# Kernel optimization log

Measured on AMD Instinct MI355X. Metric: run time of the kernel, lower is better.

The kernel has to match this reference:

```python
import jax, jax.numpy as jnp
import numpy as np

P_THRESH = 20  # p=0.2 * 100
# direction -> (di, dj): masked pixel (i,j) writes input[i,j] to x[i+di, j+dj], then avg to x[i,j]
OFFSETS = {0: (-1, -1), 1: (-1, 0), 2: (-1, 1), 3: (0, -1), 4: (0, 0), 5: (0, 1), 6: (1, -1), 7: (1, 0)}


def _shift(a, di, dj):
    """out[i+di, j+dj] = a[i, j] on last two axes; out-of-range -> 0/False."""
    H, W = a.shape[-2], a.shape[-1]
    pad = [(0, 0)] * (a.ndim - 2) + [(max(di, 0), max(-di, 0)), (max(dj, 0), max(-dj, 0))]
    p = jnp.pad(a, pad)
    sh, sw = max(-di, 0), max(-dj, 0)
    return p[..., sh:sh + H, sw:sw + W]


def _avg3x3_reflect(x):
    H, W = x.shape[-2], x.shape[-1]
    p = jnp.pad(x, [(0, 0), (0, 0), (1, 1), (1, 1)], mode='reflect')
    s = jnp.zeros_like(x)
    for i in range(3):
        for j in range(3):
            s = s + p[..., i:i + H, j:j + W]
    return s / 9.0


def brown_forward(input, dir, prob):
    avg = _avg3x3_reflect(input)
    pos = prob <= P_THRESH
    x = input
    for d in range(8):  # sequential, matching torch in-place write order
        di, dj = OFFSETS[d]
        m = (dir == d) & pos
        if d == 4:
            x = jnp.where(m, avg, x)  # mm: only avg write
        else:
            sm = _shift(m, di, dj)                       # neighbor-target mask
            x = jnp.where(sm, _shift(input, di, dj), x)  # x[i+di,j+dj] = input[i,j]
            mv = _shift(sm, -di, -dj)                    # mask restricted to valid region
            x = jnp.where(mv, avg, x)                    # x[i,j] = avg[i,j]
    return x


def setup_inputs() -> dict:
    key = jax.random.key(0)
    k1, k2, k3 = jax.random.split(key, 3)
    shape = (32, 64, 128, 128)
    return {
        'input': jax.random.normal(k1, shape, dtype=jnp.float32),
        'dir': jax.random.randint(k2, shape, 0, 8, dtype=jnp.int32),
        'prob': jax.random.randint(k3, shape, 1, 100, dtype=jnp.int32),
    }


def reference(input, dir, prob):
    return brown_forward(input, dir, prob)
```

## Files before the change

kernel.cpp:

```cpp
#include <hip/hip_runtime.h>
#include <cstddef>

#define H 128
#define W 128
#define P_THRESH 20

typedef float f4u __attribute__((ext_vector_type(4), aligned(4)));
typedef int   i4u __attribute__((ext_vector_type(4), aligned(4)));
typedef float nf2 __attribute__((ext_vector_type(2)));

__global__ __launch_bounds__(256, 6)
void brown_kernel(const float* __restrict__ inp,
                  const int*  __restrict__ dirp,
                  const int*  __restrict__ prb,
                  float* __restrict__ out)
{
    const int tid  = threadIdx.x;
    const int lane = tid & 63;
    const int bid  = blockIdx.x;
    const int slice = bid >> 5;
    const int gi   = ((bid & 31) << 2) | (tid >> 6);
    const size_t base = (size_t)slice * (size_t)(H * W);

    const int j0 = lane << 1;
    const int cl = (lane == 0) ? 0 : ((lane == 63) ? (W - 4) : (j0 - 1));

    const int rT = (gi == 0) ? 1 : gi - 1;
    const int rB = (gi == H - 1) ? H - 2 : gi + 1;

    const float* ip = inp  + base;
    const int*   dp = dirp + base;
    const int*   pp = prb  + base;

    const f4u iT = *(const f4u*)(ip + (size_t)rT * W + cl);
    const f4u iM = *(const f4u*)(ip + (size_t)gi * W + cl);
    const f4u iB = *(const f4u*)(ip + (size_t)rB * W + cl);
    const i4u dT = *(const i4u*)(dp + (size_t)rT * W + cl);
    const i4u dM = *(const i4u*)(dp + (size_t)gi * W + cl);
    const i4u dB = *(const i4u*)(dp + (size_t)rB * W + cl);
    const i4u pT = *(const i4u*)(pp + (size_t)rT * W + cl);
    const i4u pM = *(const i4u*)(pp + (size_t)gi * W + cl);
    const i4u pB = *(const i4u*)(pp + (size_t)rB * W + cl);

    auto packm = [](i4u d, i4u p) -> unsigned {
        const unsigned a = (p.x <= P_THRESH) ? (unsigned)d.x : 8u;
        const unsigned b = (p.y <= P_THRESH) ? (unsigned)d.y : 8u;
        const unsigned c = (p.z <= P_THRESH) ? (unsigned)d.z : 8u;
        const unsigned e = (p.w <= P_THRESH) ? (unsigned)d.w : 8u;
        return a | (b << 8) | (c << 16) | (e << 24);
    };
    unsigned mT = packm(dT, pT);
    unsigned mM = packm(dM, pM);
    unsigned mB = packm(dB, pB);

    if (gi == 0) {
        mT = 0x08080808u;
        unsigned r = 0;
        #pragma unroll
        for (int i2 = 0; i2 < 4; ++i2) {
            unsigned b = (mM >> (8 * i2)) & 255u;
            b = (b <= 2u) ? 8u : b;
            r |= b << (8 * i2);
        }
        mM = r;
    } else if (gi == H - 1) {
        mB = 0x08080808u;
        unsigned r = 0;
        #pragma unroll
        for (int i2 = 0; i2 < 4; ++i2) {
            unsigned b = (mM >> (8 * i2)) & 255u;
            b = (b >= 6u) ? 8u : b;
            r |= b << (8 * i2);
        }
        mM = r;
    }

    float vT[4] = {iT.x, iT.y, iT.z, iT.w};
    float vM[4] = {iM.x, iM.y, iM.z, iM.w};
    float vB[4] = {iB.x, iB.y, iB.z, iB.w};
    if (lane == 0) {
        vT[0] = iT.y; vT[1] = iT.x; vT[2] = iT.y; vT[3] = iT.z;
        vM[0] = iM.y; vM[1] = iM.x; vM[2] = iM.y; vM[3] = iM.z;
        vB[0] = iB.y; vB[1] = iB.x; vB[2] = iB.y; vB[3] = iB.z;
        mT = (mT << 8) | 8u;
        mB = (mB << 8) | 8u;
        mM = (mM << 8) | 8u;
        const unsigned b1 = (mM >> 8) & 255u;
        if ((0x49u >> b1) & 1u) mM = (mM & ~0xFF00u) | (8u << 8);
    } else if (lane == 63) {
        vT[0] = iT.y; vT[1] = iT.z; vT[2] = iT.w; vT[3] = iT.z;
        vM[0] = iM.y; vM[1] = iM.z; vM[2] = iM.w; vM[3] = iM.z;
        vB[0] = iB.y; vB[1] = iB.z; vB[2] = iB.w; vB[3] = iB.z;
        mT = (mT >> 8) | 0x08000000u;
        mB = (mB >> 8) | 0x08000000u;
        mM = (mM >> 8) | 0x08000000u;
        const unsigned b2 = (mM >> 16) & 255u;
        if ((0x24u >> b2) & 1u) mM = (mM & ~0xFF0000u) | (8u << 16);
    }

    float cs[4];
    #pragma unroll
    for (int w = 0; w < 4; ++w) cs[w] = vT[w] + vM[w] + vB[w];

    nf2 res;
    #pragma unroll
    for (int p = 0; p < 2; ++p) {
        const float avg = (cs[p] + cs[p + 1] + cs[p + 2]) * (1.0f / 9.0f);
        const unsigned wT = mT >> (8 * p);
        const unsigned wM = mM >> (8 * p);
        const unsigned wB = mB >> (8 * p);

        float val = vM[p + 1];
        int dl = -1;
        if (((wB >> 16) & 255u) == 0u) { val = vB[p + 2]; dl = 0; }
        if (((wB >>  8) & 255u) == 1u) { val = vB[p + 1]; dl = 1; }
        if (( wB        & 255u) == 2u) { val = vB[p];     dl = 2; }
        if (((wM >> 16) & 255u) == 3u) { val = vM[p + 2]; dl = 3; }
        if (( wM        & 255u) == 5u) { val = vM[p];     dl = 5; }
        if (((wT >> 16) & 255u) == 6u) { val = vT[p + 2]; dl = 6; }
        if (((wT >>  8) & 255u) == 7u) { val = vT[p + 1]; dl = 7; }

        const int msel = (int)((wM >> 8) & 255u);
        if ((msel < 8) & (msel >= dl)) val = avg;
        res[p] = val;
    }
    *(nf2*)(out + base + (size_t)gi * W + j0) = res;
}

extern "C" void kernel_launch(void* const* d_in, const int* in_sizes, int n_in,
                              void* d_out, int out_size, void* d_ws, size_t ws_size,
                              hipStream_t stream) {
    const float* inp  = (const float*)d_in[0];
    const int*   dirp = (const int*)d_in[1];
    const int*   prb  = (const int*)d_in[2];
    float* out = (float*)d_out;

    const int slices = in_sizes[0] / (H * W);
    const int grid = slices * 32;
    brown_kernel<<<grid, 256, 0, stream>>>(inp, dirp, prb, out);
}
```

Measured before the change: 397.2 us.

## Stage packed dir/prob masks in shared memory to cut redundant halo loads

Each block now loads the dir and prob rows it needs (its 4 rows plus one halo row above and below) once, with coalesced 16-byte loads, and packs them into byte masks in LDS. Threads then read their 3x3 mask neighborhood from shared memory instead of each thread re-reading three overlapping rows of dir and prob from global memory. Boundary and edge-lane handling moves into the packing stage, and edge-lane value shuffles become branchless selects. Launch bounds are raised to 8 blocks per CU. This cuts redundant global traffic and instruction count, at the cost of a __syncthreads and some unaligned LDS reads.

```diff
diff --git a/kernel.cpp b/kernel.cpp
--- a/kernel.cpp
+++ b/kernel.cpp
@@ -9,93 +9,103 @@
 typedef int   i4u __attribute__((ext_vector_type(4), aligned(4)));
 typedef float nf2 __attribute__((ext_vector_type(2)));
 
-__global__ __launch_bounds__(256, 6)
+__global__ __launch_bounds__(256, 8)
 void brown_kernel(const float* __restrict__ inp,
                   const int*  __restrict__ dirp,
                   const int*  __restrict__ prb,
                   float* __restrict__ out)
 {
-    const int tid  = threadIdx.x;
-    const int lane = tid & 63;
-    const int bid  = blockIdx.x;
+    __shared__ unsigned int s_mk[1 + 6 * 33];
+
+    const int tid   = threadIdx.x;
+    const int bid   = blockIdx.x;
     const int slice = bid >> 5;
-    const int gi   = ((bid & 31) << 2) | (tid >> 6);
+    const int r0    = (bid & 31) << 2;
     const size_t base = (size_t)slice * (size_t)(H * W);
 
-    const int j0 = lane << 1;
+    const int lane = tid & 63;
+    const int row  = tid >> 6;
+    const int gi   = r0 + row;
+    const int j0   = lane << 1;
+
     const int cl = (lane == 0) ? 0 : ((lane == 63) ? (W - 4) : (j0 - 1));
-
     const int rT = (gi == 0) ? 1 : gi - 1;
     const int rB = (gi == H - 1) ? H - 2 : gi + 1;
-
-    const float* ip = inp  + base;
-    const int*   dp = dirp + base;
-    const int*   pp = prb  + base;
-
+    const float* ip = inp + base;
     const f4u iT = *(const f4u*)(ip + (size_t)rT * W + cl);
     const f4u iM = *(const f4u*)(ip + (size_t)gi * W + cl);
     const f4u iB = *(const f4u*)(ip + (size_t)rB * W + cl);
-    const i4u dT = *(const i4u*)(dp + (size_t)rT * W + cl);
-    const i4u dM = *(const i4u*)(dp + (size_t)gi * W + cl);
-    const i4u dB = *(const i4u*)(dp + (size_t)rB * W + cl);
-    const i4u pT = *(const i4u*)(pp + (size_t)rT * W + cl);
-    const i4u pM = *(const i4u*)(pp + (size_t)gi * W + cl);
-    const i4u pB = *(const i4u*)(pp + (size_t)rB * W + cl);
 
-    auto packm = [](i4u d, i4u p) -> unsigned {
-        const unsigned a = (p.x <= P_THRESH) ? (unsigned)d.x : 8u;
-        const unsigned b = (p.y <= P_THRESH) ? (unsigned)d.y : 8u;
-        const unsigned c = (p.z <= P_THRESH) ? (unsigned)d.z : 8u;
-        const unsigned e = (p.w <= P_THRESH) ? (unsigned)d.w : 8u;
-        return a | (b << 8) | (c << 16) | (e << 24);
-    };
-    unsigned mT = packm(dT, pT);
-    unsigned mM = packm(dM, pM);
-    unsigned mB = packm(dB, pB);
+    if (tid < 192) {
+        const int r6 = tid >> 5;
+        const int w  = tid & 31;
+        const int gr = r0 + r6 - 1;
+        unsigned m;
+        if ((unsigned)gr < (unsigned)H) {
+            const i4u dv = *(const i4u*)(dirp + base + (size_t)gr * W + 4 * w);
+            const i4u pv = *(const i4u*)(prb  + base + (size_t)gr * W + 4 * w);
+            const unsigned a = (pv.x <= P_THRESH) ? (unsigned)dv.x : 8u;
+            const unsigned b = (pv.y <= P_THRESH) ? (unsigned)dv.y : 8u;
+            const unsigned c = (pv.z <= P_THRESH) ? (unsigned)dv.z : 8u;
+            const unsigned e = (pv.w <= P_THRESH) ? (unsigned)dv.w : 8u;
+            m = a | (b << 8) | (c << 16) | (e << 24);
+            if (gr == 0) {
+                unsigned mm = 0;
+                #pragma unroll
+                for (int i2 = 0; i2 < 4; ++i2) {
+                    unsigned bb = (m >> (8 * i2)) & 255u;
+                    bb = (bb <= 2u) ? 8u : bb;
+                    mm |= bb << (8 * i2);
+                }
+                m = mm;
+            } else if (gr == H - 1) {
+                unsigned mm = 0;
+                #pragma unroll
+                for (int i2 = 0; i2 < 4; ++i2) {
+                    unsigned bb = (m >> (8 * i2)) & 255u;
+                    bb = (bb >= 6u) ? 8u : bb;
+                    mm |= bb << (8 * i2);
+                }
+                m = mm;
+            }
+            if (w == 0) {
+                const unsigned b0 = m & 255u;
+                if ((0x49u >> b0) & 1u) m = (m & ~255u) | 8u;
+            }
+            if (w == 31) {
+                const unsigned b3 = m >> 24;
+                if ((0x24u >> b3) & 1u) m = (m & 0x00FFFFFFu) | (8u << 24);
+            }
+        } else {
+            m = 0x08080808u;
+        }
+        s_mk[1 + 33 * r6 + w] = m;
+        if (w == 31) s_mk[1 + 33 * r6 + 32] = 0x08080808u;
+    } else if (tid == 192) {
+        s_mk[0] = 0x08080808u;
+    }
+    __syncthreads();
 
-    if (gi == 0) {
-        mT = 0x08080808u;
-        unsigned r = 0;
-        #pragma unroll
-        for (int i2 = 0; i2 < 4; ++i2) {
-            unsigned b = (mM >> (8 * i2)) & 255u;
-            b = (b <= 2u) ? 8u : b;
-            r |= b << (8 * i2);
-        }
-        mM = r;
-    } else if (gi == H - 1) {
-        mB = 0x08080808u;
-        unsigned r = 0;
-        #pragma unroll
-        for (int i2 = 0; i2 < 4; ++i2) {
-            unsigned b = (mM >> (8 * i2)) & 255u;
-            b = (b >= 6u) ? 8u : b;
-            r |= b << (8 * i2);
-        }
-        mM = r;
+    unsigned mrow[3];
+    #pragma unroll
+    for (int dr = 0; dr < 3; ++dr) {
+        const int addr = 132 * (row + dr) + (j0 + 3);
+        const unsigned w0 = s_mk[addr >> 2];
+        const unsigned w1 = s_mk[(addr >> 2) + 1];
+        const int sh = 8 * (addr & 3);
+        mrow[dr] = (w0 >> sh) | (w1 << (32 - sh));
     }
+    const unsigned mT = mrow[0], mM = mrow[1], mB = mrow[2];
 
-    float vT[4] = {iT.x, iT.y, iT.z, iT.w};
-    float vM[4] = {iM.x, iM.y, iM.z, iM.w};
-    float vB[4] = {iB.x, iB.y, iB.z, iB.w};
-    if (lane == 0) {
-        vT[0] = iT.y; vT[1] = iT.x; vT[2] = iT.y; vT[3] = iT.z;
-        vM[0] = iM.y; vM[1] = iM.x; vM[2] = iM.y; vM[3] = iM.z;
-        vB[0] = iB.y; vB[1] = iB.x; vB[2] = iB.y; vB[3] = iB.z;
-        mT = (mT << 8) | 8u;
-        mB = (mB << 8) | 8u;
-        mM = (mM << 8) | 8u;
-        const unsigned b1 = (mM >> 8) & 255u;
-        if ((0x49u >> b1) & 1u) mM = (mM & ~0xFF00u) | (8u << 8);
-    } else if (lane == 63) {
-        vT[0] = iT.y; vT[1] = iT.z; vT[2] = iT.w; vT[3] = iT.z;
-        vM[0] = iM.y; vM[1] = iM.z; vM[2] = iM.w; vM[3] = iM.z;
-        vB[0] = iB.y; vB[1] = iB.z; vB[2] = iB.w; vB[3] = iB.z;
-        mT = (mT >> 8) | 0x08000000u;
-        mB = (mB >> 8) | 0x08000000u;
-        mM = (mM >> 8) | 0x08000000u;
-        const unsigned b2 = (mM >> 16) & 255u;
-        if ((0x24u >> b2) & 1u) mM = (mM & ~0xFF0000u) | (8u << 16);
+    const bool e0 = (lane == 0), e63 = (lane == 63), eE = e0 | e63;
+    float vT[4], vM[4], vB[4];
+    {
+        vT[0] = eE ? iT.y : iT.x;  vT[1] = e0 ? iT.x : (e63 ? iT.z : iT.y);
+        vT[2] = e0 ? iT.y : (e63 ? iT.w : iT.z);  vT[3] = eE ? iT.z : iT.w;
+        vM[0] = eE ? iM.y : iM.x;  vM[1] = e0 ? iM.x : (e63 ? iM.z : iM.y);
+        vM[2] = e0 ? iM.y : (e63 ? iM.w : iM.z);  vM[3] = eE ? iM.z : iM.w;
+        vB[0] = eE ? iB.y : iB.x;  vB[1] = e0 ? iB.x : (e63 ? iB.z : iB.y);
+        vB[2] = e0 ? iB.y : (e63 ? iB.w : iB.z);  vB[3] = eE ? iB.z : iB.w;
     }
 
     float cs[4];
```

Measured after the change: 379.6 us. 4.4% less time.
